# Kernel tuning notes

Hardware: AMD Instinct MI355X
Metric: run time of the kernel (lower is better)

Reference implementation:

```python
import jax, jax.numpy as jnp
import numpy as np

D = 1024      # hidden_dim
E = 8         # num_experts
H = 4096      # expert_hidden_dim (= 4*D, module default)
K = 2         # top-k experts per token


def setup_inputs() -> dict:
    key = jax.random.key(0)
    ks = jax.random.split(key, 7)
    s = 1.0 / np.sqrt(D)
    sh = 1.0 / np.sqrt(H)
    return {
        "x": jax.random.normal(ks[0], (4, 1024, D), dtype=jnp.float32),
        "W1": jax.random.uniform(ks[1], (E, D, H), jnp.float32, -s, s),
        "b1": jax.random.uniform(ks[2], (E, H), jnp.float32, -s, s),
        "W2": jax.random.uniform(ks[3], (E, H, D), jnp.float32, -sh, sh),
        "b2": jax.random.uniform(ks[4], (E, D), jnp.float32, -sh, sh),
        "Wg": jax.random.uniform(ks[5], (D, E), jnp.float32, -s, s),
        "bg": jax.random.uniform(ks[6], (E,), jnp.float32, -s, s),
    }


def reference(x, W1, b1, W2, b2, Wg, bg):
    orig_shape = x.shape
    x2d = x.reshape(-1, D)                                    # [N, D]
    gate_scores = jax.nn.softmax(x2d @ Wg + bg, axis=-1)      # [N, E]
    topk_scores, topk_idx = jax.lax.top_k(gate_scores, K)     # [N, K]
    # Dense all-experts 2-layer MLP (dropout is identity in eval mode)
    h = jax.nn.gelu(jnp.einsum('nd,edh->neh', x2d, W1) + b1[None], approximate=False)  # [N, E, H]
    expert_out = jnp.einsum('neh,ehd->ned', h, W2) + b2[None]  # [N, E, D]
    # Gather top-k expert outputs and combine with gate weights
    topk_out = jnp.take_along_axis(expert_out, topk_idx[:, :, None], axis=1)  # [N, K, D]
    out = jnp.sum(topk_out * topk_scores[:, :, None], axis=1)  # [N, D]
    return out.reshape(orig_shape)
```

## Files before the change

### kernel.cpp

```cpp
#include <hip/hip_runtime.h>
#include <math.h>

#define DIM  1024
#define NEXP 8
#define HID  4096
#define TOPK 2

typedef __attribute__((ext_vector_type(8))) short bf16x8;
typedef __attribute__((ext_vector_type(4))) float f32x4;

__device__ inline unsigned short f2bf(float f) {
  union { float f; unsigned int u; } v; v.f = f;
  unsigned int u = v.u;
  return (unsigned short)((u + 0x7FFFu + ((u >> 16) & 1u)) >> 16);
}

__device__ inline void load_lds16(const void* g, void* l) {
  __builtin_amdgcn_global_load_lds(
      (const __attribute__((address_space(1))) void*)g,
      (__attribute__((address_space(3))) void*)l, 16, 0, 0);
}

__global__ void gate_kernel(const float* __restrict__ x,
                            const float* __restrict__ Wg,
                            const float* __restrict__ bg,
                            float* __restrict__ topk_score,
                            int* __restrict__ count,
                            int* __restrict__ lists,
                            int N) {
  int n = blockIdx.x;
  if (n >= N) return;
  int lane = threadIdx.x;
  float acc[NEXP];
#pragma unroll
  for (int e = 0; e < NEXP; ++e) acc[e] = 0.f;
  const float* xr = x + (size_t)n * DIM;
  for (int d = lane; d < DIM; d += 64) {
    float xv = xr[d];
    const float* w = Wg + (size_t)d * NEXP;
#pragma unroll
    for (int e = 0; e < NEXP; ++e) acc[e] += xv * w[e];
  }
#pragma unroll
  for (int off = 32; off > 0; off >>= 1) {
#pragma unroll
    for (int e = 0; e < NEXP; ++e) acc[e] += __shfl_xor(acc[e], off, 64);
  }
  if (lane == 0) {
    float l[NEXP];
#pragma unroll
    for (int e = 0; e < NEXP; ++e) l[e] = acc[e] + bg[e];
    float m = l[0];
#pragma unroll
    for (int e = 1; e < NEXP; ++e) m = fmaxf(m, l[e]);
    float p[NEXP];
    float s = 0.f;
#pragma unroll
    for (int e = 0; e < NEXP; ++e) { p[e] = expf(l[e] - m); s += p[e]; }
    int i0 = 0;
#pragma unroll
    for (int e = 1; e < NEXP; ++e) if (l[e] > l[i0]) i0 = e;
    int i1 = (i0 == 0) ? 1 : 0;
#pragma unroll
    for (int e = 0; e < NEXP; ++e) if (e != i0 && l[e] > l[i1]) i1 = e;
    float inv = 1.f / s;
    topk_score[n * TOPK + 0] = p[i0] * inv;
    topk_score[n * TOPK + 1] = p[i1] * inv;
    int pos0 = atomicAdd(&count[i0], 1);
    lists[(size_t)i0 * N + pos0] = n * TOPK + 0;
    int pos1 = atomicAdd(&count[i1], 1);
    lists[(size_t)i1 * N + pos1] = n * TOPK + 1;
  }
}

__global__ void offsets_kernel(const int* __restrict__ count, int* __restrict__ offsets,
                               int* __restrict__ tiles, int* __restrict__ ntiles) {
  if (threadIdx.x == 0 && blockIdx.x == 0) {
    int s = 0, nt = 0;
    for (int e = 0; e < NEXP; ++e) {
      offsets[e] = s;
      int c = count[e];
      s += c;
      int rts = (c + 255) >> 8;
      for (int i = 0; i < rts; ++i) tiles[nt++] = (e << 16) | i;
    }
    offsets[NEXP] = s;
    ntiles[0] = nt;
  }
}

template <int TILED>
__global__ void gather_kernel(const float* __restrict__ x,
                              const int* __restrict__ offsets,
                              const int* __restrict__ lists,
                              unsigned short* __restrict__ Xg,
                              int* __restrict__ pairmap,
                              int N, int NPAD) {
  int g = blockIdx.x;
  int e = 0;
  while (e < NEXP - 1 && g >= offsets[e + 1]) ++e;
  int i = g - offsets[e];
  int ent = lists[(size_t)e * N + i];
  int tok = ent >> 1;
  if (threadIdx.x == 0) pairmap[g] = ent;
  int d0 = threadIdx.x * 4;
  float4 v = *((const float4*)(x + (size_t)tok * DIM + d0));
  ushort4 o;
  o.x = f2bf(v.x); o.y = f2bf(v.y); o.z = f2bf(v.z); o.w = f2bf(v.w);
  if (TILED) {
    *(ushort4*)(Xg + ((size_t)(d0 >> 6) * NPAD + g) * 64 + (d0 & 63)) = o;
  } else {
    *(ushort4*)(Xg + (size_t)g * DIM + d0) = o;
  }
}

__global__ __launch_bounds__(256) void transpose_convert_t(
    const float* __restrict__ src, unsigned short* __restrict__ dst, int R, int C) {
  const int e = blockIdx.z;
  src += (size_t)e * R * C;
  dst += (size_t)e * R * C;
  const int r0 = blockIdx.x * 64, c0 = blockIdx.y * 64;
  __shared__ unsigned short Ts[64][68];
  const int t = threadIdx.x;
  const int rr = t >> 4, cc = (t & 15) * 4;
#pragma unroll
  for (int p = 0; p < 4; ++p) {
    int r = rr + p * 16;
    float4 v = *(const float4*)(src + (size_t)(r0 + r) * C + c0 + cc);
    Ts[cc + 0][r] = f2bf(v.x);
    Ts[cc + 1][r] = f2bf(v.y);
    Ts[cc + 2][r] = f2bf(v.z);
    Ts[cc + 3][r] = f2bf(v.w);
  }
  __syncthreads();
  const int cr = t >> 3, rq = (t & 7) * 8;
  const size_t kbbase = (size_t)(r0 >> 6) * C;
#pragma unroll
  for (int p = 0; p < 2; ++p) {
    int c = cr + p * 32;
    ushort4 a = *(ushort4*)&Ts[c][rq];
    ushort4 b = *(ushort4*)&Ts[c][rq + 4];
    unsigned short* dp = dst + (kbbase + (c0 + c)) * 64 + rq;
    *(ushort4*)(dp) = a;
    *(ushort4*)(dp + 4) = b;
  }
}

template <int PASS>
__global__ __launch_bounds__(512, 2) void moe_gemm9(
    const unsigned short* __restrict__ Asrc,
    const unsigned short* __restrict__ Bt,
    const float* __restrict__ bias,
    const int* __restrict__ offsets,
    const int* __restrict__ tiles,
    const int* __restrict__ ntiles,
    const int* __restrict__ pairmap,
    const float* __restrict__ score,
    unsigned short* __restrict__ Hmat,
    float* __restrict__ out,
    int maxt, int NPAD) {
  constexpr int K  = (PASS == 1) ? DIM : HID;
  constexpr int NS = (PASS == 1) ? HID : DIM;
  constexpr int KS = (PASS == 1) ? 1 : 2;
  constexpr int KL = K / KS;
  constexpr int NT = KL / 64;
  constexpr int KBK = K / 64;

  const unsigned orig = blockIdx.x;
  const unsigned nwg = gridDim.x;
  const unsigned q = nwg >> 3, r8 = nwg & 7;
  const unsigned xcd = orig & 7, p8 = orig >> 3;
  const unsigned id = (xcd < r8 ? xcd * (q + 1) : r8 * (q + 1) + (xcd - r8) * q) + p8;
  const int tt = (int)(id % (unsigned)maxt);
  const int ct = (int)(id / (unsigned)maxt);

  if (tt >= ntiles[0]) return;
  const int pk = tiles[tt];
  const int e  = pk >> 16;
  const int rt = pk & 0xffff;
  const int gbase = offsets[e];
  const int nc = offsets[e + 1] - gbase;
  const int rowsvalid = min(256, nc - rt * 256);
  const int kz = (PASS == 1) ? 0 : blockIdx.z;
  const int kb0 = (kz * KL) >> 6;

  __shared__ unsigned short As[3][16384];
  __shared__ unsigned short Bs[3][8192];

  const int tid  = threadIdx.x;
  const int lane = tid & 63;
  const int wid  = tid >> 6;
  const int wr = (wid >> 1) * 64;
  const int wc = (wid & 1) * 64;
  const int fr = lane & 15;
  const int fq = lane >> 4;

  f32x4 acc[4][4];
#pragma unroll
  for (int m = 0; m < 4; ++m)
#pragma unroll
    for (int n = 0; n < 4; ++n) acc[m][n] = (f32x4){0.f, 0.f, 0.f, 0.f};

  const unsigned short* Ab = Asrc + ((size_t)kb0 * NPAD + (gbase + rt * 256)) * 64;
  const unsigned short* Bb = Bt + (((size_t)e * KBK + kb0) * NS + (size_t)ct * 128) * 64;

  auto stage = [&](int b, int t) {
    const unsigned short* ga = Ab + (size_t)t * ((size_t)NPAD * 64);
    const unsigned short* gb = Bb + (size_t)t * ((size_t)NS * 64);
#pragma unroll
    for (int i = 0; i < 4; ++i) {
      const int c = i * 512 + tid;
      const int off = ((c >> 3) * 8 + ((c & 7) ^ ((c >> 3) & 7))) * 8;
      load_lds16(ga + off, (char*)As[b] + c * 16);
    }
#pragma unroll
    for (int i = 0; i < 2; ++i) {
      const int c = i * 512 + tid;
      const int off = ((c >> 3) * 8 + ((c & 7) ^ ((c >> 3) & 7))) * 8;
      load_lds16(gb + off, (char*)Bs[b] + c * 16);
    }
  };

  stage(0, 0);
  stage(1, 1);

  for (int t = 0; t < NT; ++t) {
    if (t + 2 < NT) {
      stage((t + 2) % 3, t + 2);
      asm volatile("s_waitcnt vmcnt(12)" ::: "memory");
    } else if (t + 2 == NT) {
      asm volatile("s_waitcnt vmcnt(6)" ::: "memory");
    } else {
      asm volatile("s_waitcnt vmcnt(0)" ::: "memory");
    }
    __builtin_amdgcn_s_barrier();

    const unsigned short* Ac = As[t % 3];
    const unsigned short* Bc = Bs[t % 3];
#pragma unroll
    for (int kk = 0; kk < 2; ++kk) {
      bf16x8 af[4], bf[4];
#pragma unroll
      for (int m = 0; m < 4; ++m) {
        const int row = wr + m * 16 + fr;
        const int u = (kk * 4 + fq) ^ (row & 7);
        af[m] = *(const bf16x8*)&Ac[row * 64 + u * 8];
      }
#pragma unroll
      for (int n = 0; n < 4; ++n) {
        const int row = wc + n * 16 + fr;
        const int u = (kk * 4 + fq) ^ (row & 7);
        bf[n] = *(const bf16x8*)&Bc[row * 64 + u * 8];
      }
      __builtin_amdgcn_s_setprio(1);
#pragma unroll
      for (int m = 0; m < 4; ++m)
#pragma unroll
        for (int n = 0; n < 4; ++n)
          acc[m][n] = __builtin_amdgcn_mfma_f32_16x16x32_bf16(af[m], bf[n], acc[m][n], 0, 0, 0);
      __builtin_amdgcn_s_setprio(0);
    }
    __builtin_amdgcn_s_barrier();
  }

  if (PASS == 1) {
    const size_t cb = (size_t)(ct * 2 + (wc >> 6));
#pragma unroll
    for (int n = 0; n < 4; ++n) {
      const int col = ct * 128 + wc + n * 16 + fr;
      const int cl = n * 16 + fr;
      const float b1v = bias[(size_t)e * NS + col];
#pragma unroll
      for (int m = 0; m < 4; ++m) {
#pragma unroll
        for (int r = 0; r < 4; ++r) {
          const int lrow = wr + m * 16 + fq * 4 + r;
          if (lrow < rowsvalid) {
            float v = acc[m][n][r] + b1v;
            v = 0.5f * v * (1.f + erff(v * 0.70710678118654752440f));
            Hmat[(cb * NPAD + (gbase + rt * 256 + lrow)) * 64 + cl] = f2bf(v);
          }
        }
      }
    }
  } else {
    float b2v[4];
#pragma unroll
    for (int n = 0; n < 4; ++n)
      b2v[n] = (kz == 0) ? bias[(size_t)e * NS + ct * 128 + wc + n * 16 + fr] : 0.f;
#pragma unroll
    for (int m = 0; m < 4; ++m) {
#pragma unroll
      for (int r = 0; r < 4; ++r) {
        const int lrow = wr + m * 16 + fq * 4 + r;
        if (lrow < rowsvalid) {
          const int g = gbase + rt * 256 + lrow;
          const int ent = pairmap[g];
          const int tok = ent >> 1;
          const float s = score[ent];
#pragma unroll
          for (int n = 0; n < 4; ++n) {
            const int col = ct * 128 + wc + n * 16 + fr;
            atomicAdd(&out[(size_t)tok * DIM + col], s * (acc[m][n][r] + b2v[n]));
          }
        }
      }
    }
  }
}

template <int PASS>
__global__ __launch_bounds__(256) void moe_gemm(
    const unsigned short* __restrict__ Asrc,
    const float* __restrict__ Bsrc,
    const float* __restrict__ bias,
    const int* __restrict__ offsets,
    const int* __restrict__ pairmap,
    const float* __restrict__ score,
    unsigned short* __restrict__ Hmat,
    float* __restrict__ out) {
  constexpr int K  = (PASS == 1) ? DIM : HID;
  constexpr int NS = (PASS == 1) ? HID : DIM;
  const int e = blockIdx.z;
  const int gbase = offsets[e];
  const int nc = offsets[e + 1] - gbase;
  const int rt = blockIdx.x;
  if (rt * 128 >= nc) return;
  const int rowsvalid = min(128, nc - rt * 128);
  const int ct = blockIdx.y;
  __shared__ unsigned short As[128 * 40];
  __shared__ unsigned short Bs[128 * 40];
  const int tid  = threadIdx.x;
  const int lane = tid & 63;
  const int wid  = tid >> 6;
  const int wr = (wid >> 1) * 64;
  const int wc = (wid & 1) * 64;
  const int fr = lane & 15;
  const int fq = lane >> 4;
  f32x4 acc[4][4];
#pragma unroll
  for (int m = 0; m < 4; ++m)
#pragma unroll
    for (int n = 0; n < 4; ++n) acc[m][n] = (f32x4){0.f, 0.f, 0.f, 0.f};
  const int ar = tid >> 1;
  const int ak = (tid & 1) * 16;
  int arow = rt * 128 + ((ar < rowsvalid) ? ar : 0);
  const unsigned short* Aptr = Asrc + (size_t)(gbase + arow) * K + ak;
  const int bc = (tid & 31) * 4;
  const int bk = (tid >> 5) * 4;
  const float* Bptr = Bsrc + (size_t)e * K * NS + (size_t)bk * NS + ct * 128 + bc;
  for (int k0 = 0; k0 < K; k0 += 32) {
    uint4 av0 = *(const uint4*)(Aptr + k0);
    uint4 av1 = *(const uint4*)(Aptr + k0 + 8);
    const float* bp = Bptr + (size_t)k0 * NS;
    float4 w0 = *(const float4*)(bp);
    float4 w1 = *(const float4*)(bp + NS);
    float4 w2 = *(const float4*)(bp + 2 * NS);
    float4 w3 = *(const float4*)(bp + 3 * NS);
    __syncthreads();
    *(uint4*)&As[ar * 40 + ak]     = av0;
    *(uint4*)&As[ar * 40 + ak + 8] = av1;
    {
      uint2 pv;
      pv.x = (unsigned int)f2bf(w0.x) | ((unsigned int)f2bf(w1.x) << 16);
      pv.y = (unsigned int)f2bf(w2.x) | ((unsigned int)f2bf(w3.x) << 16);
      *(uint2*)&Bs[(bc + 0) * 40 + bk] = pv;
      pv.x = (unsigned int)f2bf(w0.y) | ((unsigned int)f2bf(w1.y) << 16);
      pv.y = (unsigned int)f2bf(w2.y) | ((unsigned int)f2bf(w3.y) << 16);
      *(uint2*)&Bs[(bc + 1) * 40 + bk] = pv;
      pv.x = (unsigned int)f2bf(w0.z) | ((unsigned int)f2bf(w1.z) << 16);
      pv.y = (unsigned int)f2bf(w2.z) | ((unsigned int)f2bf(w3.z) << 16);
      *(uint2*)&Bs[(bc + 2) * 40 + bk] = pv;
      pv.x = (unsigned int)f2bf(w0.w) | ((unsigned int)f2bf(w1.w) << 16);
      pv.y = (unsigned int)f2bf(w2.w) | ((unsigned int)f2bf(w3.w) << 16);
      *(uint2*)&Bs[(bc + 3) * 40 + bk] = pv;
    }
    __syncthreads();
    bf16x8 af[4], bfr[4];
#pragma unroll
    for (int m = 0; m < 4; ++m)
      af[m] = *(const bf16x8*)&As[(wr + m * 16 + fr) * 40 + fq * 8];
#pragma unroll
    for (int n = 0; n < 4; ++n)
      bfr[n] = *(const bf16x8*)&Bs[(wc + n * 16 + fr) * 40 + fq * 8];
#pragma unroll
    for (int m = 0; m < 4; ++m)
#pragma unroll
      for (int n = 0; n < 4; ++n)
        acc[m][n] = __builtin_amdgcn_mfma_f32_16x16x32_bf16(af[m], bfr[n], acc[m][n], 0, 0, 0);
  }
  if (PASS == 1) {
#pragma unroll
    for (int n = 0; n < 4; ++n) {
      int col = ct * 128 + wc + n * 16 + fr;
      float b1v = bias[(size_t)e * NS + col];
#pragma unroll
      for (int m = 0; m < 4; ++m) {
#pragma unroll
        for (int r = 0; r < 4; ++r) {
          int lrow = wr + m * 16 + fq * 4 + r;
          if (lrow < rowsvalid) {
            float v = acc[m][n][r] + b1v;
            v = 0.5f * v * (1.f + erff(v * 0.70710678118654752440f));
            Hmat[(size_t)(gbase + rt * 128 + lrow) * HID + col] = f2bf(v);
          }
        }
      }
    }
  } else {
    float b2v[4];
#pragma unroll
    for (int n = 0; n < 4; ++n)
      b2v[n] = bias[(size_t)e * NS + ct * 128 + wc + n * 16 + fr];
#pragma unroll
    for (int m = 0; m < 4; ++m) {
#pragma unroll
      for (int r = 0; r < 4; ++r) {
        int lrow = wr + m * 16 + fq * 4 + r;
        if (lrow < rowsvalid) {
          int g = gbase + rt * 128 + lrow;
          int ent = pairmap[g];
          int tok = ent >> 1;
          float s = score[ent];
#pragma unroll
          for (int n = 0; n < 4; ++n) {
            int col = ct * 128 + wc + n * 16 + fr;
            atomicAdd(&out[(size_t)tok * DIM + col], s * (acc[m][n][r] + b2v[n]));
          }
        }
      }
    }
  }
}

extern "C" void kernel_launch(void* const* d_in, const int* in_sizes, int n_in,
                              void* d_out, int out_size, void* d_ws, size_t ws_size,
                              hipStream_t stream) {
  const float* x  = (const float*)d_in[0];
  const float* W1 = (const float*)d_in[1];
  const float* b1 = (const float*)d_in[2];
  const float* W2 = (const float*)d_in[3];
  const float* b2 = (const float*)d_in[4];
  const float* Wg = (const float*)d_in[5];
  const float* bg = (const float*)d_in[6];
  float* out = (float*)d_out;
  const int N  = in_sizes[0] / DIM;
  const int NP = N * TOPK;
  const int NPAD = NP + 256;
  const int MAXT = NP / 256 + NEXP;

  char* ws = (char*)d_ws;
  size_t off = 0;
  auto alloc = [&](size_t bytes) -> void* {
    void* p = ws + off;
    off = (off + bytes + 255) & ~(size_t)255;
    return p;
  };
  int*   count      = (int*)alloc(NEXP * sizeof(int));
  int*   offsets    = (int*)alloc((NEXP + 1) * sizeof(int));
  int*   tiles      = (int*)alloc((size_t)MAXT * sizeof(int));
  int*   ntiles     = (int*)alloc(sizeof(int));
  float* topk_score = (float*)alloc((size_t)NP * sizeof(float));
  int*   lists      = (int*)alloc((size_t)NEXP * N * sizeof(int));
  int*   pairmap    = (int*)alloc((size_t)NP * sizeof(int));
  unsigned short* Xg   = (unsigned short*)alloc((size_t)NPAD * DIM * sizeof(unsigned short));
  unsigned short* Hmat = (unsigned short*)alloc((size_t)NPAD * HID * sizeof(unsigned short));
  unsigned short* W1T = (unsigned short*)alloc((size_t)NEXP * DIM * HID * sizeof(unsigned short));
  unsigned short* W2T = (unsigned short*)alloc((size_t)NEXP * HID * DIM * sizeof(unsigned short));
  size_t need_full = off;

  hipMemsetAsync(count, 0, NEXP * sizeof(int), stream);
  gate_kernel<<<N, 64, 0, stream>>>(x, Wg, bg, topk_score, count, lists, N);
  offsets_kernel<<<1, 64, 0, stream>>>(count, offsets, tiles, ntiles);
  hipMemsetAsync(out, 0, (size_t)out_size * sizeof(float), stream);

  if (ws_size >= need_full) {
    gather_kernel<1><<<NP, DIM / 4, 0, stream>>>(x, offsets, lists, Xg, pairmap, N, NPAD);
    dim3 tg1(DIM / 64, HID / 64, NEXP);
    transpose_convert_t<<<tg1, 256, 0, stream>>>(W1, W1T, DIM, HID);
    dim3 tg2(HID / 64, DIM / 64, NEXP);
    transpose_convert_t<<<tg2, 256, 0, stream>>>(W2, W2T, HID, DIM);

    dim3 g1((HID / 128) * MAXT, 1, 1);
    moe_gemm9<1><<<g1, 512, 0, stream>>>(Xg, W1T, b1, offsets, tiles, ntiles,
                                         pairmap, topk_score, Hmat, out, MAXT, NPAD);
    dim3 g2((DIM / 128) * MAXT, 1, 2);
    moe_gemm9<2><<<g2, 512, 0, stream>>>(Hmat, W2T, b2, offsets, tiles, ntiles,
                                         pairmap, topk_score, Hmat, out, MAXT, NPAD);
  } else {
    gather_kernel<0><<<NP, DIM / 4, 0, stream>>>(x, offsets, lists, Xg, pairmap, N, NPAD);
    const int RT = (N + 127) / 128;
    dim3 g1(RT, HID / 128, NEXP);
    moe_gemm<1><<<g1, 256, 0, stream>>>(Xg, W1, b1, offsets, pairmap, topk_score, Hmat, out);
    dim3 g2(RT, DIM / 128, NEXP);
    moe_gemm<2><<<g2, 256, 0, stream>>>(Hmat, W2, b2, offsets, pairmap, topk_score, Hmat, out);
  }
}
```

Before: 593.3 us.

## Shrink expert GEMM tiles to 128x128 with single-buffered unswizzled LDS

Replaces the 256x128 triple-buffered MoE GEMM (512 threads) with a 128x128 tile using 256 threads, a single LDS buffer per operand loaded synchronously each k-step, and no XOR swizzle or priority hints. Row tiles per expert become 128 rows, which reduces padding waste and raises the tile count for load balance. In exchange it drops the load/compute overlap, reintroduces LDS bank conflicts on fragment reads, and halves B-tile reuse per block.

```diff
diff --git a/kernel.cpp b/kernel.cpp
--- a/kernel.cpp
+++ b/kernel.cpp
@@ -81,7 +81,7 @@
       offsets[e] = s;
       int c = count[e];
       s += c;
-      int rts = (c + 255) >> 8;
+      int rts = (c + 127) >> 7;
       for (int i = 0; i < rts; ++i) tiles[nt++] = (e << 16) | i;
     }
     offsets[NEXP] = s;
@@ -147,7 +147,7 @@
 }
 
 template <int PASS>
-__global__ __launch_bounds__(512, 2) void moe_gemm9(
+__global__ __launch_bounds__(256) void moe_gemm10(
     const unsigned short* __restrict__ Asrc,
     const unsigned short* __restrict__ Bt,
     const float* __restrict__ bias,
@@ -180,12 +180,12 @@
   const int rt = pk & 0xffff;
   const int gbase = offsets[e];
   const int nc = offsets[e + 1] - gbase;
-  const int rowsvalid = min(256, nc - rt * 256);
+  const int rowsvalid = min(128, nc - rt * 128);
   const int kz = (PASS == 1) ? 0 : blockIdx.z;
   const int kb0 = (kz * KL) >> 6;
 
-  __shared__ unsigned short As[3][16384];
-  __shared__ unsigned short Bs[3][8192];
+  __shared__ unsigned short As[128 * 64];
+  __shared__ unsigned short Bs[128 * 64];
 
   const int tid  = threadIdx.x;
   const int lane = tid & 63;
@@ -201,66 +201,38 @@
 #pragma unroll
     for (int n = 0; n < 4; ++n) acc[m][n] = (f32x4){0.f, 0.f, 0.f, 0.f};
 
-  const unsigned short* Ab = Asrc + ((size_t)kb0 * NPAD + (gbase + rt * 256)) * 64;
+  const unsigned short* Ab = Asrc + ((size_t)kb0 * NPAD + (gbase + rt * 128)) * 64;
   const unsigned short* Bb = Bt + (((size_t)e * KBK + kb0) * NS + (size_t)ct * 128) * 64;
 
-  auto stage = [&](int b, int t) {
-    const unsigned short* ga = Ab + (size_t)t * ((size_t)NPAD * 64);
-    const unsigned short* gb = Bb + (size_t)t * ((size_t)NS * 64);
-#pragma unroll
-    for (int i = 0; i < 4; ++i) {
-      const int c = i * 512 + tid;
-      const int off = ((c >> 3) * 8 + ((c & 7) ^ ((c >> 3) & 7))) * 8;
-      load_lds16(ga + off, (char*)As[b] + c * 16);
-    }
-#pragma unroll
-    for (int i = 0; i < 2; ++i) {
-      const int c = i * 512 + tid;
-      const int off = ((c >> 3) * 8 + ((c & 7) ^ ((c >> 3) & 7))) * 8;
-      load_lds16(gb + off, (char*)Bs[b] + c * 16);
-    }
-  };
-
-  stage(0, 0);
-  stage(1, 1);
-
   for (int t = 0; t < NT; ++t) {
-    if (t + 2 < NT) {
-      stage((t + 2) % 3, t + 2);
-      asm volatile("s_waitcnt vmcnt(12)" ::: "memory");
-    } else if (t + 2 == NT) {
-      asm volatile("s_waitcnt vmcnt(6)" ::: "memory");
-    } else {
-      asm volatile("s_waitcnt vmcnt(0)" ::: "memory");
-    }
-    __builtin_amdgcn_s_barrier();
-
-    const unsigned short* Ac = As[t % 3];
-    const unsigned short* Bc = Bs[t % 3];
+    {
+      const unsigned short* ga = Ab + (size_t)t * ((size_t)NPAD * 64);
+      const unsigned short* gb = Bb + (size_t)t * ((size_t)NS * 64);
+#pragma unroll
+      for (int i = 0; i < 4; ++i) {
+        const int c = i * 256 + tid;
+        load_lds16(ga + c * 8, (char*)As + c * 16);
+        load_lds16(gb + c * 8, (char*)Bs + c * 16);
+      }
+    }
+    __syncthreads();
+
 #pragma unroll
     for (int kk = 0; kk < 2; ++kk) {
       bf16x8 af[4], bf[4];
 #pragma unroll
-      for (int m = 0; m < 4; ++m) {
-        const int row = wr + m * 16 + fr;
-        const int u = (kk * 4 + fq) ^ (row & 7);
-        af[m] = *(const bf16x8*)&Ac[row * 64 + u * 8];
-      }
-#pragma unroll
-      for (int n = 0; n < 4; ++n) {
-        const int row = wc + n * 16 + fr;
-        const int u = (kk * 4 + fq) ^ (row & 7);
-        bf[n] = *(const bf16x8*)&Bc[row * 64 + u * 8];
-      }
-      __builtin_amdgcn_s_setprio(1);
+      for (int m = 0; m < 4; ++m)
+        af[m] = *(const bf16x8*)&As[(wr + m * 16 + fr) * 64 + (kk * 4 + fq) * 8];
+#pragma unroll
+      for (int n = 0; n < 4; ++n)
+        bf[n] = *(const bf16x8*)&Bs[(wc + n * 16 + fr) * 64 + (kk * 4 + fq) * 8];
 #pragma unroll
       for (int m = 0; m < 4; ++m)
 #pragma unroll
         for (int n = 0; n < 4; ++n)
           acc[m][n] = __builtin_amdgcn_mfma_f32_16x16x32_bf16(af[m], bf[n], acc[m][n], 0, 0, 0);
-      __builtin_amdgcn_s_setprio(0);
-    }
-    __builtin_amdgcn_s_barrier();
+    }
+    __syncthreads();
   }
 
   if (PASS == 1) {
@@ -278,7 +250,7 @@
           if (lrow < rowsvalid) {
             float v = acc[m][n][r] + b1v;
             v = 0.5f * v * (1.f + erff(v * 0.70710678118654752440f));
-            Hmat[(cb * NPAD + (gbase + rt * 256 + lrow)) * 64 + cl] = f2bf(v);
+            Hmat[(cb * NPAD + (gbase + rt * 128 + lrow)) * 64 + cl] = f2bf(v);
           }
         }
       }
@@ -294,7 +266,7 @@
       for (int r = 0; r < 4; ++r) {
         const int lrow = wr + m * 16 + fq * 4 + r;
         if (lrow < rowsvalid) {
-          const int g = gbase + rt * 256 + lrow;
+          const int g = gbase + rt * 128 + lrow;
           const int ent = pairmap[g];
           const int tok = ent >> 1;
           const float s = score[ent];
@@ -447,7 +419,7 @@
   const int N  = in_sizes[0] / DIM;
   const int NP = N * TOPK;
   const int NPAD = NP + 256;
-  const int MAXT = NP / 256 + NEXP;
+  const int MAXT = NP / 128 + NEXP;
 
   char* ws = (char*)d_ws;
   size_t off = 0;
@@ -482,11 +454,11 @@
     transpose_convert_t<<<tg2, 256, 0, stream>>>(W2, W2T, HID, DIM);
 
     dim3 g1((HID / 128) * MAXT, 1, 1);
-    moe_gemm9<1><<<g1, 512, 0, stream>>>(Xg, W1T, b1, offsets, tiles, ntiles,
-                                         pairmap, topk_score, Hmat, out, MAXT, NPAD);
+    moe_gemm10<1><<<g1, 256, 0, stream>>>(Xg, W1T, b1, offsets, tiles, ntiles,
+                                          pairmap, topk_score, Hmat, out, MAXT, NPAD);
     dim3 g2((DIM / 128) * MAXT, 1, 2);
-    moe_gemm9<2><<<g2, 512, 0, stream>>>(Hmat, W2T, b2, offsets, tiles, ntiles,
-                                         pairmap, topk_score, Hmat, out, MAXT, NPAD);
+    moe_gemm10<2><<<g2, 256, 0, stream>>>(Hmat, W2T, b2, offsets, tiles, ntiles,
+                                          pairmap, topk_score, Hmat, out, MAXT, NPAD);
   } else {
     gather_kernel<0><<<NP, DIM / 4, 0, stream>>>(x, offsets, lists, Xg, pairmap, N, NPAD);
     const int RT = (N + 127) / 128;
```

Result: faster. 523.5 us (-11.8%).
